# Optimization experiments

Hardware: AMD Instinct MI355X
Metric: run time of the kernel (lower is better)

## Reference

```python
import jax, jax.numpy as jnp
import numpy as np

R = 16  # number of attention heads


def setup_inputs() -> dict:
    key = jax.random.key(0)
    ks = jax.random.split(key, 6)
    B, T, D = 2, 2048, 1024
    s = 1.0 / np.sqrt(D)
    return {
        "q": jax.random.normal(ks[0], (B, T, D), jnp.float32),
        "k": jax.random.normal(ks[1], (B, T, D), jnp.float32),
        "q_map": jax.random.normal(ks[2], (D, D), jnp.float32) * s,
        "k_map": jax.random.normal(ks[3], (D, D), jnp.float32) * s,
        "v_map": jax.random.normal(ks[4], (D, D), jnp.float32) * s,
        "output_map": jax.random.normal(ks[5], (D, D), jnp.float32) * s,
    }


def _split_heads(x, r):
    # [B, T, D] -> [B, r, T, D//r]
    B, T, D = x.shape
    return x.reshape(B, T, r, D // r).transpose(0, 2, 1, 3)


def reference(q, k, q_map, k_map, v_map, output_map):
    # v = k (the layer reuses Keys as Values)
    B, Tq, D = q.shape
    dh = D // R
    qh = _split_heads(q @ q_map, R)  # [B, r, Tq, dh]
    kh = _split_heads(k @ k_map, R)  # [B, r, Tk, dh]
    vh = _split_heads(k @ v_map, R)  # [B, r, Tk, dh]
    scale = 1.0 / jnp.sqrt(jnp.asarray(dh, qh.dtype))
    scores = jnp.einsum('brqd,brkd->brqk', qh, kh) * scale
    weights = jax.nn.softmax(scores, axis=-1)  # dropout=0 / inference -> identity
    out = jnp.einsum('brqk,brkd->brqd', weights, vh)  # [B, r, Tq, dh]
    merged = out.transpose(0, 2, 1, 3).reshape(B, Tq, D)
    return merged @ output_map
```

## Files before the change

kernel.cpp:

```cpp
#include <hip/hip_runtime.h>
#include <hip/hip_bf16.h>


typedef unsigned short u16;
typedef __attribute__((ext_vector_type(8))) short short8;
typedef __attribute__((ext_vector_type(4))) float f32x4;

__device__ __forceinline__ u16 f2bf(float f) {
  __hip_bfloat16 h = __float2bfloat16(f);
  return reinterpret_cast<u16&>(h);
}

__device__ __forceinline__ void gl_lds16(const u16* g, u16* l) {
  __builtin_amdgcn_global_load_lds(
      (const __attribute__((address_space(1))) void*)g,
      (__attribute__((address_space(3))) void*)l, 16, 0, 0);
}

template <int ROWS>
__device__ __forceinline__ void stage_tile(const u16* __restrict__ g, int gs,
                                           u16* lds, int wave, int lane) {
  const int lr8 = lane >> 3;
  const int gc = ((lane & 7) ^ lr8) * 8;
#pragma unroll
  for (int w = 0; w < ROWS / 32; ++w) {
    int t = w * 4 + wave;
    gl_lds16(g + (size_t)(t * 8 + lr8) * gs + gc, lds + t * 512);
  }
}

__global__ __launch_bounds__(256)
void convert_qk(const float4* __restrict__ q, const float4* __restrict__ k,
                u16* __restrict__ qb, u16* __restrict__ kb) {
  int i = blockIdx.x * 256 + threadIdx.x;
  float4 qv = q[i], kv = k[i];
  ushort4 qo, ko;
  qo.x = f2bf(qv.x); qo.y = f2bf(qv.y); qo.z = f2bf(qv.z); qo.w = f2bf(qv.w);
  ko.x = f2bf(kv.x); ko.y = f2bf(kv.y); ko.z = f2bf(kv.z); ko.w = f2bf(kv.w);
  reinterpret_cast<ushort4*>(qb)[i] = qo;
  reinterpret_cast<ushort4*>(kb)[i] = ko;
}

__global__ __launch_bounds__(256)
void convert_maps(const float* __restrict__ qm, const float* __restrict__ km,
                  const float* __restrict__ vm, const float* __restrict__ om,
                  u16* __restrict__ qmT, u16* __restrict__ kmT,
                  u16* __restrict__ vmT, u16* __restrict__ omT) {
  __shared__ float t[32][33];
  const float* src; u16* dst; float scale = 1.0f;
  switch (blockIdx.z) {
    case 0:  src = qm; dst = qmT; scale = 0.125f; break;
    case 1:  src = km; dst = kmT; break;
    case 2:  src = vm; dst = vmT; break;
    default: src = om; dst = omT; break;
  }
  int nb0 = blockIdx.x * 32, kb0 = blockIdx.y * 32;
  int c = threadIdx.x & 31, rq = threadIdx.x >> 5;
#pragma unroll
  for (int j = 0; j < 4; ++j)
    t[rq * 4 + j][c] = src[(size_t)(kb0 + rq * 4 + j) * 1024 + nb0 + c];
  __syncthreads();
#pragma unroll
  for (int j = 0; j < 4; ++j) {
    int nn = rq * 4 + j;
    dst[(size_t)(nb0 + nn) * 1024 + kb0 + c] = f2bf(t[c][nn] * scale);
  }
}

__global__ __launch_bounds__(256)
void gemm_qkv(const u16* __restrict__ qb, const u16* __restrict__ kb,
              const u16* __restrict__ Bt, u16* __restrict__ Qp,
              u16* __restrict__ Kp, u16* __restrict__ Vt) {
  __shared__ u16 As[2][128 * 64];
  __shared__ u16 Bs[2][128 * 64];
  const int tid = threadIdx.x;
  const int wave = tid >> 6, lane = tid & 63;
  const int lr = lane & 15, lg = lane >> 4;
  const int xx = blockIdx.x;
  const int m0 = blockIdx.y * 128, n0 = xx * 128;
  const int wm = (wave >> 1) * 64, wn = (wave & 1) * 64;
  const u16* A = (xx < 8) ? qb : kb;

  f32x4 acc[4][4] = {};
  const int K = 1024;
  const u16* Ab = A + (size_t)m0 * K;
  const u16* Bb = Bt + (size_t)n0 * K;

  stage_tile<128>(Ab, K, &As[0][0], wave, lane);
  stage_tile<128>(Bb, K, &Bs[0][0], wave, lane);
  __syncthreads();

  int cur = 0;
  for (int kt = 0; kt < 16; ++kt) {
    if (kt + 1 < 16) {
      stage_tile<128>(Ab + (kt + 1) * 64, K, &As[cur ^ 1][0], wave, lane);
      stage_tile<128>(Bb + (kt + 1) * 64, K, &Bs[cur ^ 1][0], wave, lane);
    }
#pragma unroll
    for (int ks = 0; ks < 2; ++ks) {
      short8 af[4], bfr[4];
#pragma unroll
      for (int i = 0; i < 4; ++i) {
        int ar = wm + i * 16 + lr;
        int ac = (ks * 4 + lg) ^ (ar & 7);
        af[i] = *reinterpret_cast<const short8*>(&As[cur][ar * 64 + ac * 8]);
      }
#pragma unroll
      for (int j = 0; j < 4; ++j) {
        int br = wn + j * 16 + lr;
        int bc = (ks * 4 + lg) ^ (br & 7);
        bfr[j] = *reinterpret_cast<const short8*>(&Bs[cur][br * 64 + bc * 8]);
      }
#pragma unroll
      for (int i = 0; i < 4; ++i)
#pragma unroll
        for (int j = 0; j < 4; ++j)
          acc[i][j] = __builtin_amdgcn_mfma_f32_16x16x32_bf16(af[i], bfr[j], acc[i][j], 0, 0, 0);
    }
    __syncthreads();
    cur ^= 1;
  }

#pragma unroll
  for (int i = 0; i < 4; ++i) {
    int row0 = m0 + wm + i * 16 + lg * 4;
#pragma unroll
    for (int j = 0; j < 4; ++j) {
      int col = n0 + wn + j * 16 + lr;
      if (xx < 8) {
#pragma unroll
        for (int r = 0; r < 4; ++r)
          Qp[(size_t)(row0 + r) * 1024 + col] = f2bf(acc[i][j][r]);
      } else if (xx < 16) {
#pragma unroll
        for (int r = 0; r < 4; ++r)
          Kp[(size_t)(row0 + r) * 1024 + (col - 1024)] = f2bf(acc[i][j][r]);
      } else {
        int bb = row0 >> 11, kk = row0 & 2047;
        int hd = col - 2048;
        uint2 pk;
        pk.x = (unsigned)f2bf(acc[i][j][0]) | ((unsigned)f2bf(acc[i][j][1]) << 16);
        pk.y = (unsigned)f2bf(acc[i][j][2]) | ((unsigned)f2bf(acc[i][j][3]) << 16);
        *reinterpret_cast<uint2*>(&Vt[(size_t)(bb * 1024 + hd) * 2048 + kk]) = pk;
      }
    }
  }
}

__global__ __launch_bounds__(256)
void gemm_out(const u16* __restrict__ A, const u16* __restrict__ Bt,
              float* __restrict__ C, int K, int ldc) {
  __shared__ u16 As[2][128 * 64];
  __shared__ u16 Bs[2][64 * 64];
  const int tid = threadIdx.x;
  const int wave = tid >> 6, lane = tid & 63;
  const int lr = lane & 15, lg = lane >> 4;
  const int m0 = blockIdx.y * 128, n0 = blockIdx.x * 64;
  const int wm = (wave >> 1) * 64, wn = (wave & 1) * 32;

  f32x4 acc[4][2] = {};
  const int kT = K >> 6;
  const u16* Ab = A + (size_t)m0 * K;
  const u16* Bb = Bt + (size_t)n0 * K;

  stage_tile<128>(Ab, K, &As[0][0], wave, lane);
  stage_tile<64>(Bb, K, &Bs[0][0], wave, lane);
  __syncthreads();

  int cur = 0;
  for (int kt = 0; kt < kT; ++kt) {
    if (kt + 1 < kT) {
      stage_tile<128>(Ab + (kt + 1) * 64, K, &As[cur ^ 1][0], wave, lane);
      stage_tile<64>(Bb + (kt + 1) * 64, K, &Bs[cur ^ 1][0], wave, lane);
    }
#pragma unroll
    for (int ks = 0; ks < 2; ++ks) {
      short8 af[4], bfr[2];
#pragma unroll
      for (int i = 0; i < 4; ++i) {
        int ar = wm + i * 16 + lr;
        int ac = (ks * 4 + lg) ^ (ar & 7);
        af[i] = *reinterpret_cast<const short8*>(&As[cur][ar * 64 + ac * 8]);
      }
#pragma unroll
      for (int j = 0; j < 2; ++j) {
        int br = wn + j * 16 + lr;
        int bc = (ks * 4 + lg) ^ (br & 7);
        bfr[j] = *reinterpret_cast<const short8*>(&Bs[cur][br * 64 + bc * 8]);
      }
#pragma unroll
      for (int i = 0; i < 4; ++i)
#pragma unroll
        for (int j = 0; j < 2; ++j)
          acc[i][j] = __builtin_amdgcn_mfma_f32_16x16x32_bf16(af[i], bfr[j], acc[i][j], 0, 0, 0);
    }
    __syncthreads();
    cur ^= 1;
  }
#pragma unroll
  for (int i = 0; i < 4; ++i) {
    int row0 = m0 + wm + i * 16 + lg * 4;
#pragma unroll
    for (int j = 0; j < 2; ++j) {
      int col = n0 + wn + j * 16 + lr;
#pragma unroll
      for (int r = 0; r < 4; ++r)
        C[(size_t)(row0 + r) * ldc + col] = acc[i][j][r];
    }
  }
}

__global__ __launch_bounds__(256)
void attention(const u16* __restrict__ Qp, const u16* __restrict__ Kp,
               const u16* __restrict__ Vt, u16* __restrict__ merged) {
  __shared__ u16 Ks[2][64 * 64];
  __shared__ u16 Vs[2][64 * 64];
  const int tid = threadIdx.x;
  const int wave = tid >> 6, lane = tid & 63;
  const int lr = lane & 15, lg = lane >> 4;
  const int qt = blockIdx.x, h = blockIdx.y, b = blockIdx.z;
  const int q0 = qt * 64;

  short8 qf[2];
  const size_t qrow = (size_t)(b * 2048 + q0 + wave * 16 + lr);
  qf[0] = *reinterpret_cast<const short8*>(&Qp[qrow * 1024 + h * 64 + lg * 8]);
  qf[1] = *reinterpret_cast<const short8*>(&Qp[qrow * 1024 + h * 64 + 32 + lg * 8]);

  f32x4 oacc[4] = {};
  float ell = 0.f;

  const u16* Kg = Kp + (size_t)(b * 2048) * 1024 + h * 64;
  const u16* Vg = Vt + (size_t)(b * 1024 + h * 64) * 2048;

  stage_tile<64>(Kg, 1024, &Ks[0][0], wave, lane);
  stage_tile<64>(Vg, 2048, &Vs[0][0], wave, lane);
  __syncthreads();

  int cur = 0;
  for (int ktile = 0; ktile < 32; ++ktile) {
    if (ktile + 1 < 32) {
      const int kn = (ktile + 1) * 64;
      stage_tile<64>(Kg + (size_t)kn * 1024, 1024, &Ks[cur ^ 1][0], wave, lane);
      stage_tile<64>(Vg + kn, 2048, &Vs[cur ^ 1][0], wave, lane);
    }
    unsigned W[4][2];
#pragma unroll
    for (int kf = 0; kf < 4; ++kf) {
      f32x4 z = {};
#pragma unroll
      for (int ks = 0; ks < 2; ++ks) {
        int br = kf * 16 + lr;
        int bc = (ks * 4 + lg) ^ (br & 7);
        short8 kbf = *reinterpret_cast<const short8*>(&Ks[cur][br * 64 + bc * 8]);
        z = __builtin_amdgcn_mfma_f32_16x16x32_bf16(kbf, qf[ks], z, 0, 0, 0);
      }
      float p0 = __expf(z[0]), p1 = __expf(z[1]);
      float p2 = __expf(z[2]), p3 = __expf(z[3]);
      ell += (p0 + p1) + (p2 + p3);
      W[kf][0] = (unsigned)f2bf(p0) | ((unsigned)f2bf(p1) << 16);
      W[kf][1] = (unsigned)f2bf(p2) | ((unsigned)f2bf(p3) << 16);
    }
    const int src01 = lr + ((lg & 1) << 5);
    const int src23 = src01 + 16;
    const bool hiq = lg >= 2;
#pragma unroll
    for (int ks = 0; ks < 2; ++ks) {
      unsigned lo0 = (unsigned)__shfl((int)W[ks * 2][0],     src01);
      unsigned hi0 = (unsigned)__shfl((int)W[ks * 2 + 1][0], src01);
      unsigned lo1 = (unsigned)__shfl((int)W[ks * 2][1],     src01);
      unsigned hi1 = (unsigned)__shfl((int)W[ks * 2 + 1][1], src01);
      unsigned lo2 = (unsigned)__shfl((int)W[ks * 2][0],     src23);
      unsigned hi2 = (unsigned)__shfl((int)W[ks * 2 + 1][0], src23);
      unsigned lo3 = (unsigned)__shfl((int)W[ks * 2][1],     src23);
      unsigned hi3 = (unsigned)__shfl((int)W[ks * 2 + 1][1], src23);
      union { uint4 u; short8 s; } pu;
      pu.u.x = hiq ? hi0 : lo0;
      pu.u.y = hiq ? hi1 : lo1;
      pu.u.z = hiq ? hi2 : lo2;
      pu.u.w = hiq ? hi3 : lo3;
#pragma unroll
      for (int df = 0; df < 4; ++df) {
        int vr = df * 16 + lr;
        int vc = (ks * 4 + lg) ^ (vr & 7);
        short8 vb = *reinterpret_cast<const short8*>(&Vs[cur][vr * 64 + vc * 8]);
        oacc[df] = __builtin_amdgcn_mfma_f32_16x16x32_bf16(pu.s, vb, oacc[df], 0, 0, 0);
      }
    }
    __syncthreads();
    cur ^= 1;
  }
  float e = ell;
  e += __shfl_xor(e, 16);
  e += __shfl_xor(e, 32);
  float inv = 1.0f / e;
  float invr[4];
#pragma unroll
  for (int r = 0; r < 4; ++r) invr[r] = __shfl(inv, lg * 4 + r);
  const size_t rowbase = (size_t)(b * 2048 + q0 + wave * 16 + lg * 4);
#pragma unroll
  for (int df = 0; df < 4; ++df)
#pragma unroll
    for (int r = 0; r < 4; ++r)
      merged[(rowbase + r) * 1024 + h * 64 + df * 16 + lr] =
          f2bf(oacc[df][r] * invr[r]);
}

extern "C" void kernel_launch(void* const* d_in, const int* in_sizes, int n_in,
                              void* d_out, int out_size, void* d_ws, size_t ws_size,
                              hipStream_t stream) {
  const float* q  = (const float*)d_in[0];
  const float* k  = (const float*)d_in[1];
  const float* qm = (const float*)d_in[2];
  const float* km = (const float*)d_in[3];
  const float* vm = (const float*)d_in[4];
  const float* om = (const float*)d_in[5];
  float* out = (float*)d_out;

  char* w = (char*)d_ws;
  const size_t MB = 1024 * 1024;
  u16* qb  = (u16*)(w + 0 * MB);
  u16* kb  = (u16*)(w + 8 * MB);
  u16* qmT = (u16*)(w + 16 * MB);
  u16* kmT = (u16*)(w + 18 * MB);
  u16* vmT = (u16*)(w + 20 * MB);
  u16* omT = (u16*)(w + 22 * MB);
  u16* Qp  = (u16*)(w + 24 * MB);
  u16* Kp  = (u16*)(w + 32 * MB);
  u16* Vt  = (u16*)(w + 48 * MB);
  u16* merged = qb;

  convert_qk<<<4096, 256, 0, stream>>>((const float4*)q, (const float4*)k, qb, kb);
  convert_maps<<<dim3(32, 32, 4), 256, 0, stream>>>(qm, km, vm, om, qmT, kmT, vmT, omT);
  gemm_qkv<<<dim3(24, 32), 256, 0, stream>>>(qb, kb, qmT, Qp, Kp, Vt);
  attention<<<dim3(32, 16, 2), 256, 0, stream>>>(Qp, Kp, Vt, merged);
  gemm_out<<<dim3(16, 32), 256, 0, stream>>>(merged, omT, out, 1024, 1024);
}
```

Baseline: 242.9 us.

## Double query rows per attention block and pass P through LDS

Each attention block now handles 128 query rows instead of 64, with each wave holding two 16-row query fragments. Each staged K/V tile is therefore reused across twice as many queries, which halves K/V global and LDS traffic per query. The permutation of the probability fragments, previously done with register shuffles, now goes through a per-wave LDS buffer. The grid shrinks to 512 blocks, which may lower occupancy and adds register and LDS pressure.

```diff
diff --git a/kernel.cpp b/kernel.cpp
--- a/kernel.cpp
+++ b/kernel.cpp
@@ -215,19 +215,25 @@
                const u16* __restrict__ Vt, u16* __restrict__ merged) {
   __shared__ u16 Ks[2][64 * 64];
   __shared__ u16 Vs[2][64 * 64];
+  __shared__ unsigned Pbuf[8][512];
   const int tid = threadIdx.x;
   const int wave = tid >> 6, lane = tid & 63;
   const int lr = lane & 15, lg = lane >> 4;
   const int qt = blockIdx.x, h = blockIdx.y, b = blockIdx.z;
-  const int q0 = qt * 64;
-
-  short8 qf[2];
-  const size_t qrow = (size_t)(b * 2048 + q0 + wave * 16 + lr);
-  qf[0] = *reinterpret_cast<const short8*>(&Qp[qrow * 1024 + h * 64 + lg * 8]);
-  qf[1] = *reinterpret_cast<const short8*>(&Qp[qrow * 1024 + h * 64 + 32 + lg * 8]);
-
-  f32x4 oacc[4] = {};
-  float ell = 0.f;
+  const int q0 = qt * 128;
+
+  short8 qf[2][2];
+#pragma unroll
+  for (int qm = 0; qm < 2; ++qm) {
+    const size_t qrow = (size_t)(b * 2048 + q0 + wave * 32 + qm * 16 + lr);
+#pragma unroll
+    for (int ks = 0; ks < 2; ++ks)
+      qf[qm][ks] = *reinterpret_cast<const short8*>(
+          &Qp[qrow * 1024 + h * 64 + ks * 32 + lg * 8]);
+  }
+
+  f32x4 oacc[2][4] = {};
+  float ell[2] = {0.f, 0.f};
 
   const u16* Kg = Kp + (size_t)(b * 2048) * 1024 + h * 64;
   const u16* Vg = Vt + (size_t)(b * 1024 + h * 64) * 2048;
@@ -243,66 +249,73 @@
       stage_tile<64>(Kg + (size_t)kn * 1024, 1024, &Ks[cur ^ 1][0], wave, lane);
       stage_tile<64>(Vg + kn, 2048, &Vs[cur ^ 1][0], wave, lane);
     }
-    unsigned W[4][2];
+    short8 kfr[4][2];
 #pragma unroll
     for (int kf = 0; kf < 4; ++kf) {
-      f32x4 z = {};
+      int br = kf * 16 + lr;
 #pragma unroll
       for (int ks = 0; ks < 2; ++ks) {
-        int br = kf * 16 + lr;
         int bc = (ks * 4 + lg) ^ (br & 7);
-        short8 kbf = *reinterpret_cast<const short8*>(&Ks[cur][br * 64 + bc * 8]);
-        z = __builtin_amdgcn_mfma_f32_16x16x32_bf16(kbf, qf[ks], z, 0, 0, 0);
-      }
-      float p0 = __expf(z[0]), p1 = __expf(z[1]);
-      float p2 = __expf(z[2]), p3 = __expf(z[3]);
-      ell += (p0 + p1) + (p2 + p3);
-      W[kf][0] = (unsigned)f2bf(p0) | ((unsigned)f2bf(p1) << 16);
-      W[kf][1] = (unsigned)f2bf(p2) | ((unsigned)f2bf(p3) << 16);
-    }
-    const int src01 = lr + ((lg & 1) << 5);
-    const int src23 = src01 + 16;
-    const bool hiq = lg >= 2;
+        kfr[kf][ks] = *reinterpret_cast<const short8*>(&Ks[cur][br * 64 + bc * 8]);
+      }
+    }
+#pragma unroll
+    for (int qm = 0; qm < 2; ++qm) {
+      unsigned* Pw = &Pbuf[wave * 2 + qm][0];
+#pragma unroll
+      for (int kf = 0; kf < 4; ++kf) {
+        f32x4 z = {};
+#pragma unroll
+        for (int ks = 0; ks < 2; ++ks)
+          z = __builtin_amdgcn_mfma_f32_16x16x32_bf16(kfr[kf][ks], qf[qm][ks], z, 0, 0, 0);
+        float p0 = __expf(z[0]), p1 = __expf(z[1]);
+        float p2 = __expf(z[2]), p3 = __expf(z[3]);
+        ell[qm] += (p0 + p1) + (p2 + p3);
+        uint2 pk;
+        pk.x = (unsigned)f2bf(p0) | ((unsigned)f2bf(p1) << 16);
+        pk.y = (unsigned)f2bf(p2) | ((unsigned)f2bf(p3) << 16);
+        *reinterpret_cast<uint2*>(&Pw[((kf * 16 + lr) * 4 + lg) * 2]) = pk;
+      }
+    }
+    asm volatile("s_waitcnt lgkmcnt(0)" ::: "memory");
+    __builtin_amdgcn_sched_barrier(0);
 #pragma unroll
     for (int ks = 0; ks < 2; ++ks) {
-      unsigned lo0 = (unsigned)__shfl((int)W[ks * 2][0],     src01);
-      unsigned hi0 = (unsigned)__shfl((int)W[ks * 2 + 1][0], src01);
-      unsigned lo1 = (unsigned)__shfl((int)W[ks * 2][1],     src01);
-      unsigned hi1 = (unsigned)__shfl((int)W[ks * 2 + 1][1], src01);
-      unsigned lo2 = (unsigned)__shfl((int)W[ks * 2][0],     src23);
-      unsigned hi2 = (unsigned)__shfl((int)W[ks * 2 + 1][0], src23);
-      unsigned lo3 = (unsigned)__shfl((int)W[ks * 2][1],     src23);
-      unsigned hi3 = (unsigned)__shfl((int)W[ks * 2 + 1][1], src23);
-      union { uint4 u; short8 s; } pu;
-      pu.u.x = hiq ? hi0 : lo0;
-      pu.u.y = hiq ? hi1 : lo1;
-      pu.u.z = hiq ? hi2 : lo2;
-      pu.u.w = hiq ? hi3 : lo3;
+      short8 pa[2];
+#pragma unroll
+      for (int qm = 0; qm < 2; ++qm)
+        pa[qm] = *reinterpret_cast<const short8*>(
+            &Pbuf[wave * 2 + qm][(((ks * 2 + (lg >> 1)) * 16 + lr) * 4 + 2 * (lg & 1)) * 2]);
 #pragma unroll
       for (int df = 0; df < 4; ++df) {
         int vr = df * 16 + lr;
         int vc = (ks * 4 + lg) ^ (vr & 7);
         short8 vb = *reinterpret_cast<const short8*>(&Vs[cur][vr * 64 + vc * 8]);
-        oacc[df] = __builtin_amdgcn_mfma_f32_16x16x32_bf16(pu.s, vb, oacc[df], 0, 0, 0);
+#pragma unroll
+        for (int qm = 0; qm < 2; ++qm)
+          oacc[qm][df] = __builtin_amdgcn_mfma_f32_16x16x32_bf16(pa[qm], vb, oacc[qm][df], 0, 0, 0);
       }
     }
     __syncthreads();
     cur ^= 1;
   }
-  float e = ell;
-  e += __shfl_xor(e, 16);
-  e += __shfl_xor(e, 32);
-  float inv = 1.0f / e;
-  float invr[4];
-#pragma unroll
-  for (int r = 0; r < 4; ++r) invr[r] = __shfl(inv, lg * 4 + r);
-  const size_t rowbase = (size_t)(b * 2048 + q0 + wave * 16 + lg * 4);
-#pragma unroll
-  for (int df = 0; df < 4; ++df)
-#pragma unroll
-    for (int r = 0; r < 4; ++r)
-      merged[(rowbase + r) * 1024 + h * 64 + df * 16 + lr] =
-          f2bf(oacc[df][r] * invr[r]);
+#pragma unroll
+  for (int qm = 0; qm < 2; ++qm) {
+    float e = ell[qm];
+    e += __shfl_xor(e, 16);
+    e += __shfl_xor(e, 32);
+    float inv = 1.0f / e;
+    float invr[4];
+#pragma unroll
+    for (int r = 0; r < 4; ++r) invr[r] = __shfl(inv, lg * 4 + r);
+    const size_t rowbase = (size_t)(b * 2048 + q0 + wave * 32 + qm * 16 + lg * 4);
+#pragma unroll
+    for (int df = 0; df < 4; ++df)
+#pragma unroll
+      for (int r = 0; r < 4; ++r)
+        merged[(rowbase + r) * 1024 + h * 64 + df * 16 + lr] =
+            f2bf(oacc[qm][df][r] * invr[r]);
+  }
 }
 
 extern "C" void kernel_launch(void* const* d_in, const int* in_sizes, int n_in,
@@ -332,6 +345,6 @@
   convert_qk<<<4096, 256, 0, stream>>>((const float4*)q, (const float4*)k, qb, kb);
   convert_maps<<<dim3(32, 32, 4), 256, 0, stream>>>(qm, km, vm, om, qmT, kmT, vmT, omT);
   gemm_qkv<<<dim3(24, 32), 256, 0, stream>>>(qb, kb, qmT, Qp, Kp, Vt);
-  attention<<<dim3(32, 16, 2), 256, 0, stream>>>(Qp, Kp, Vt, merged);
+  attention<<<dim3(16, 16, 2), 256, 0, stream>>>(Qp, Kp, Vt, merged);
   gemm_out<<<dim3(16, 32), 256, 0, stream>>>(merged, omT, out, 1024, 1024);
 }
```

Result: faster. 229.3 us (-5.6%).
